# Optimization experiments

Hardware: AMD Instinct MI355X
Metric: run time of the kernel (lower is better)

The kernel has to match this reference:

```python
import jax, jax.numpy as jnp
import numpy as np

B, S, D, H, HD, I, L = 1, 2048, 1024, 16, 64, 2816, 2
EPS = 1e-5
ROPE_BASE = 10000.0


def rmsnorm(x, w):
    return x * jax.lax.rsqrt(jnp.mean(x * x, axis=-1, keepdims=True) + EPS) * w


def precompute_freqs_cis():
    # matches precompute_freqs_cis: [S, HD//2, 2] = (cos, sin)
    freqs = 1.0 / (ROPE_BASE ** (jnp.arange(0, HD, 2, dtype=jnp.float32) / HD))
    ang = jnp.outer(jnp.arange(S, dtype=jnp.float32), freqs)
    return jnp.stack([jnp.cos(ang), jnp.sin(ang)], axis=-1)


def apply_rope(x, fc):
    # x: [B,S,H,HD]; fc: [S,HD//2,2] -> interleaved pair rotation
    xs = x.reshape(*x.shape[:-1], HD // 2, 2)
    f = fc[None, :, None]  # [1,S,1,HD//2,2]
    out = jnp.stack([
        xs[..., 0] * f[..., 0] - xs[..., 1] * f[..., 1],
        xs[..., 1] * f[..., 0] + xs[..., 0] * f[..., 1],
    ], axis=-1)
    return out.reshape(x.shape)


def setup_inputs() -> dict:
    key = jax.random.key(0)
    ks = jax.random.split(key, 6)
    p = lambda k, shape: jax.random.normal(k, shape, jnp.float32) * 0.02
    return {
        "x": jax.random.normal(ks[0], (B, S, D), jnp.float32),
        "wqkv": p(ks[1], (L, 3 * H * HD, D)),
        "wo": p(ks[2], (L, D, H * HD)),
        "w1": p(ks[3], (L, I, D)),
        "w2": p(ks[4], (L, D, I)),
        "w3": p(ks[5], (L, I, D)),
        "attn_norm_w": jnp.ones((L, D), jnp.float32),
        "ffn_norm_w": jnp.ones((L, D), jnp.float32),
        "attn_ls": 0.01 * jnp.ones((L, D), jnp.float32),
        "ffn_ls": 0.01 * jnp.ones((L, D), jnp.float32),
        "final_norm_w": jnp.ones((D,), jnp.float32),
    }


def reference(x, wqkv, wo, w1, w2, w3, attn_norm_w, ffn_norm_w, attn_ls, ffn_ls, final_norm_w):
    fc = precompute_freqs_cis()
    causal = jnp.tril(jnp.ones((S, S), dtype=bool))  # [S,S]
    scale = 1.0 / np.sqrt(HD).astype(np.float32)
    h = x
    for l in range(L):
        # --- attention block ---
        xn = rmsnorm(h, attn_norm_w[l])
        qkv = xn @ wqkv[l].T  # [B,S,3*H*HD]
        q, k, v = jnp.split(qkv, 3, axis=-1)
        q = apply_rope(q.reshape(B, S, H, HD), fc)
        k = apply_rope(k.reshape(B, S, H, HD), fc)
        v = v.reshape(B, S, H, HD)
        scores = jnp.einsum('bqhd,bkhd->bhqk', q, k) * scale
        scores = jnp.where(causal, scores, jnp.finfo(scores.dtype).min)
        attn = jax.nn.softmax(scores, axis=-1)
        y = jnp.einsum('bhqk,bkhd->bqhd', attn, v).reshape(B, S, H * HD)
        h = h + (y @ wo[l].T) * attn_ls[l]
        # --- feed-forward block (SwiGLU) ---
        xn = rmsnorm(h, ffn_norm_w[l])
        ff = (jax.nn.silu(xn @ w1[l].T) * (xn @ w3[l].T)) @ w2[l].T
        h = h + ff * ffn_ls[l]
    return rmsnorm(h, final_norm_w)
```

## Files before the change

### kernel.cpp

```cpp
#include <hip/hip_runtime.h>
#include <math.h>

#define SEQ 2048
#define DIM 1024
#define NH 16
#define HDIM 64
#define IDIM 2816
#define NL 2

typedef __attribute__((ext_vector_type(8))) short bf16x8;
typedef __attribute__((ext_vector_type(4))) float f32x4;

__device__ __forceinline__ unsigned short f2bf(float f) {
    unsigned int u = __float_as_uint(f);
    u = (u + 0x7fffu + ((u >> 16) & 1u)) >> 16;
    return (unsigned short)u;
}
__device__ __forceinline__ float bf2f(unsigned short u) {
    return __uint_as_float((unsigned int)u << 16);
}

__device__ __forceinline__ void gl_lds16(const void* g, void* l) {
    __builtin_amdgcn_global_load_lds(
        (const __attribute__((address_space(1))) unsigned int*)g,
        (__attribute__((address_space(3))) unsigned int*)l, 16, 0, 0);
}

#define WAITVM(n) asm volatile("s_waitcnt vmcnt(" #n ")" ::: "memory")
#define BARRIER_PIN()                       \
    do {                                    \
        __builtin_amdgcn_s_barrier();       \
        __builtin_amdgcn_sched_barrier(0);  \
    } while (0)

template <bool BF16OUT>
__global__ __launch_bounds__(256) void rmsnorm_kernel(const float* __restrict__ in,
                                                      const float* __restrict__ w,
                                                      void* __restrict__ out) {
    const int row = blockIdx.x;
    const int t = threadIdx.x;
    const float4 v = ((const float4*)(in + (size_t)row * DIM))[t];
    float ss = v.x * v.x + v.y * v.y + v.z * v.z + v.w * v.w;
#pragma unroll
    for (int m = 1; m < 64; m <<= 1) ss += __shfl_xor(ss, m);
    __shared__ float red[4];
    if ((t & 63) == 0) red[t >> 6] = ss;
    __syncthreads();
    const float tot = red[0] + red[1] + red[2] + red[3];
    const float r = 1.0f / sqrtf(tot * (1.0f / DIM) + 1e-5f);
    const float4 wv = ((const float4*)w)[t];
    float o0 = v.x * r * wv.x, o1 = v.y * r * wv.y;
    float o2 = v.z * r * wv.z, o3 = v.w * r * wv.w;
    if (BF16OUT) {
        ushort4 o = {f2bf(o0), f2bf(o1), f2bf(o2), f2bf(o3)};
        ((ushort4*)((unsigned short*)out + (size_t)row * DIM))[t] = o;
    } else {
        float4 o = {o0, o1, o2, o3};
        ((float4*)((float*)out + (size_t)row * DIM))[t] = o;
    }
}

#define WQKV_OFF 0
#define WO_OFF   3145728
#define W1_OFF   4194304
#define W3_OFF   7077888
#define W2_OFF   9961472
#define WTOT     12845056

__global__ __launch_bounds__(256) void convert_weights_kernel(
    const float* __restrict__ wqkv, const float* __restrict__ wo,
    const float* __restrict__ w1, const float* __restrict__ w3,
    const float* __restrict__ w2, unsigned short* __restrict__ out) {
    const size_t i8 = ((size_t)blockIdx.x * 256 + threadIdx.x) * 8;
    const float* src;
    size_t local;
    if (i8 < WO_OFF)      { src = wqkv; local = i8 - WQKV_OFF; }
    else if (i8 < W1_OFF) { src = wo;   local = i8 - WO_OFF; }
    else if (i8 < W3_OFF) { src = w1;   local = i8 - W1_OFF; }
    else if (i8 < W2_OFF) { src = w3;   local = i8 - W3_OFF; }
    else                  { src = w2;   local = i8 - W2_OFF; }
    const float4 v0 = *(const float4*)(src + local);
    const float4 v1 = *(const float4*)(src + local + 4);
    ushort4 o0 = {f2bf(v0.x), f2bf(v0.y), f2bf(v0.z), f2bf(v0.w)};
    ushort4 o1 = {f2bf(v1.x), f2bf(v1.y), f2bf(v1.z), f2bf(v1.w)};
    *(ushort4*)(out + i8) = o0;
    *(ushort4*)(out + i8 + 4) = o1;
}

template <int EPI, int BM, int BN, int KSPLIT>
__global__ __launch_bounds__(256) void mfma_gemm(
    const unsigned short* __restrict__ A,
    const unsigned short* __restrict__ B,
    const unsigned short* __restrict__ Bhi, int nsplit,
    float* __restrict__ Cf,
    unsigned short* __restrict__ Cb,
    const float* __restrict__ ls,
    int N, int K) {
    constexpr int MI = BM / 32;
    constexpr int NJ = BN / 32;
    constexpr int L = BM / 64 + BN / 64;
    __shared__ unsigned short As[3][BM * 32];
    __shared__ unsigned short Bs[3][BN * 32];

    const int tid = threadIdx.x;

    const int nwg = gridDim.x * gridDim.y;
    const int orig = blockIdx.y * gridDim.x + blockIdx.x;
    const int swz = (orig & 7) * (nwg >> 3) + (orig >> 3);
    const int bx = swz % gridDim.x;
    const int by = swz / gridDim.x;
    const int m0 = by * BM;
    const int ncol0 = bx * BN;

    const unsigned short* Bp = B;
    int n0 = ncol0;
    if (n0 >= nsplit) { Bp = Bhi; n0 -= nsplit; }

    const int Koff = (KSPLIT > 1) ? blockIdx.z * (K / KSPLIT) : 0;

    const int srow = tid >> 2;
    const int skof = (tid & 3) * 8;
    const unsigned short* Ag = A + (size_t)(m0 + srow) * K + Koff + skof;
    const unsigned short* Bg = Bp + (size_t)(n0 + srow) * K + Koff + skof;

    const int lane = tid & 63;
    const int wid = tid >> 6;
    const int wr = (wid >> 1) * (BM / 2);
    const int wc = (wid & 1) * (BN / 2);
    const int fr = lane & 15;
    const int fk = (lane >> 4) * 8;

    f32x4 acc[MI][NJ] = {};

#define STAGE(buf, kk)                                                        \
    {                                                                         \
        _Pragma("unroll")                                                     \
        for (int p = 0; p < BM / 64; ++p)                                     \
            gl_lds16(Ag + (size_t)(p * 64) * K + (kk),                        \
                     &As[buf][p * 2048 + tid * 8]);                           \
        _Pragma("unroll")                                                     \
        for (int p = 0; p < BN / 64; ++p)                                     \
            gl_lds16(Bg + (size_t)(p * 64) * K + (kk),                        \
                     &Bs[buf][p * 2048 + tid * 8]);                           \
    }

    auto compute_tile = [&](int buf) {
        bf16x8 a[MI], b[NJ];
#pragma unroll
        for (int m = 0; m < MI; ++m)
            a[m] = *(const bf16x8*)&As[buf][(wr + m * 16 + fr) * 32 + fk];
#pragma unroll
        for (int n = 0; n < NJ; ++n)
            b[n] = *(const bf16x8*)&Bs[buf][(wc + n * 16 + fr) * 32 + fk];
        __builtin_amdgcn_s_setprio(1);
#pragma unroll
        for (int m = 0; m < MI; ++m)
#pragma unroll
            for (int n = 0; n < NJ; ++n)
                acc[m][n] = __builtin_amdgcn_mfma_f32_16x16x32_bf16(a[m], b[n], acc[m][n], 0, 0, 0);
        __builtin_amdgcn_s_setprio(0);
    };

    const int NT = K / KSPLIT / 32;

    STAGE(0, 0);
    STAGE(1, 32);
    STAGE(2, 64);

    int buf = 0;
    for (int t = 0; t < NT - 2; ++t) {
        if constexpr (L == 3) WAITVM(6); else WAITVM(8);
        BARRIER_PIN();
        compute_tile(buf);
        asm volatile("s_waitcnt lgkmcnt(0)" ::: "memory");
        BARRIER_PIN();
        if (t + 3 < NT) STAGE(buf, (t + 3) * 32);
        buf = (buf == 2) ? 0 : buf + 1;
    }
    if constexpr (L == 3) WAITVM(3); else WAITVM(4);
    BARRIER_PIN();
    compute_tile(buf);
    asm volatile("s_waitcnt lgkmcnt(0)" ::: "memory");
    BARRIER_PIN();
    buf = (buf == 2) ? 0 : buf + 1;
    WAITVM(0);
    BARRIER_PIN();
    compute_tile(buf);
#undef STAGE

    const int erow = m0 + wr + (lane >> 4) * 4;
    const int ecol = ncol0 + wc + fr;
#pragma unroll
    for (int m = 0; m < MI; ++m) {
#pragma unroll
        for (int n = 0; n < NJ; ++n) {
            const f32x4 v = acc[m][n];
            const int row = erow + m * 16;
            const int col = ecol + n * 16;
            if (EPI == 1) {
                const float lv = ls[col];
#pragma unroll
                for (int j = 0; j < 4; ++j) {
                    float* p = Cf + (size_t)(row + j) * N + col;
                    if (KSPLIT > 1) atomicAdd(p, v[j] * lv);
                    else            *p = *p + v[j] * lv;
                }
            } else {
#pragma unroll
                for (int j = 0; j < 4; ++j)
                    Cb[(size_t)(row + j) * N + col] = f2bf(v[j]);
            }
        }
    }
}

__global__ __launch_bounds__(256) void silu_mul_kernel(
    const unsigned short* __restrict__ c13,
    unsigned short* __restrict__ outp) {
    const size_t e8 = ((size_t)blockIdx.x * 256 + threadIdx.x) * 8;
    const int m = (int)(e8 / IDIM);
    const int i = (int)(e8 % IDIM);
    const unsigned short* g = c13 + (size_t)m * (2 * IDIM) + i;
    const bf16x8 gv = *(const bf16x8*)g;
    const bf16x8 uv = *(const bf16x8*)(g + IDIM);
    unsigned short o[8];
#pragma unroll
    for (int j = 0; j < 8; ++j) {
        const float x = bf2f((unsigned short)gv[j]);
        const float u = bf2f((unsigned short)uv[j]);
        o[j] = f2bf(x / (1.0f + __expf(-x)) * u);
    }
    *(bf16x8*)(outp + (size_t)m * IDIM + i) = *(const bf16x8*)o;
}

__global__ __launch_bounds__(256) void rope_split_kernel(
    const unsigned short* __restrict__ qkv,
    unsigned short* __restrict__ Qh,
    unsigned short* __restrict__ Kh,
    unsigned short* __restrict__ Vt) {
    const int st = blockIdx.x;
    const int h = blockIdx.y;
    const int tid = threadIdx.x;
    const int srow = tid >> 2;
    const int scol = (tid & 3) * 16;
    const int s = st * 64 + srow;
    __shared__ unsigned short Vl[64][72];

    const unsigned short* base = qkv + (size_t)s * (3 * DIM) + h * HDIM + scol;

    unsigned short qv[16], kv[16], vv[16];
    *(bf16x8*)&qv[0] = *(const bf16x8*)(base);
    *(bf16x8*)&qv[8] = *(const bf16x8*)(base + 8);
    *(bf16x8*)&kv[0] = *(const bf16x8*)(base + DIM);
    *(bf16x8*)&kv[8] = *(const bf16x8*)(base + DIM + 8);
    *(bf16x8*)&vv[0] = *(const bf16x8*)(base + 2 * DIM);
    *(bf16x8*)&vv[8] = *(const bf16x8*)(base + 2 * DIM + 8);

    unsigned short qo[16], ko[16];
#pragma unroll
    for (int i = 0; i < 8; ++i) {
        const int p = scol / 2 + i;
        const float freq = powf(10000.0f, -(float)(2 * p) * (1.0f / 64.0f));
        const float ang = (float)s * freq;
        float sn, cs;
        sincosf(ang, &sn, &cs);
        const float q0 = bf2f(qv[2 * i]), q1 = bf2f(qv[2 * i + 1]);
        const float k0 = bf2f(kv[2 * i]), k1 = bf2f(kv[2 * i + 1]);
        qo[2 * i]     = f2bf(q0 * cs - q1 * sn);
        qo[2 * i + 1] = f2bf(q1 * cs + q0 * sn);
        ko[2 * i]     = f2bf(k0 * cs - k1 * sn);
        ko[2 * i + 1] = f2bf(k1 * cs + k0 * sn);
    }
    unsigned short* qdst = Qh + ((size_t)h * SEQ + s) * HDIM + scol;
    unsigned short* kdst = Kh + ((size_t)h * SEQ + s) * HDIM + scol;
    *(bf16x8*)qdst = *(const bf16x8*)&qo[0];
    *(bf16x8*)(qdst + 8) = *(const bf16x8*)&qo[8];
    *(bf16x8*)kdst = *(const bf16x8*)&ko[0];
    *(bf16x8*)(kdst + 8) = *(const bf16x8*)&ko[8];

#pragma unroll
    for (int i = 0; i < 16; ++i) Vl[scol + i][srow] = vv[i];
    __syncthreads();
    const int d = tid >> 2;
    const int c0 = (tid & 3) * 16;
    unsigned short* vdst = Vt + ((size_t)h * HDIM + d) * SEQ + st * 64 + c0;
    *(bf16x8*)vdst = *(const bf16x8*)&Vl[d][c0];
    *(bf16x8*)(vdst + 8) = *(const bf16x8*)&Vl[d][c0 + 8];
}

__global__ __launch_bounds__(256) void attn_mfma_kernel(
    const unsigned short* __restrict__ Qh,
    const unsigned short* __restrict__ Kh,
    const unsigned short* __restrict__ Vt,
    unsigned short* __restrict__ y) {
    const int h = blockIdx.x;
    const int qt = blockIdx.y;
    const int qb = (qt < 16) ? qt : 47 - qt;

    __shared__ unsigned short Ql[64][72];
    __shared__ unsigned short Kl[2][64][72];
    __shared__ unsigned short Vl[2][64][72];
    __shared__ unsigned short Pl[64][72];

    const int tid = threadIdx.x;
    const int lane = tid & 63;
    const int w = tid >> 6;
    const int fr = lane & 15;
    const int fk = (lane >> 4) * 8;
    const int rg = (lane >> 4) * 4;
    const int srow = tid >> 2;
    const int sc8 = (tid & 3) * 8;

    {
        const unsigned short* src = Qh + ((size_t)h * SEQ + qb * 64 + srow) * HDIM + sc8;
        *(bf16x8*)&Ql[srow][sc8] = *(const bf16x8*)src;
        *(bf16x8*)&Ql[srow][sc8 + 32] = *(const bf16x8*)(src + 32);
    }
    __syncthreads();
    bf16x8 qa[2];
    qa[0] = *(const bf16x8*)&Ql[w * 16 + fr][fk];
    qa[1] = *(const bf16x8*)&Ql[w * 16 + fr][32 + fk];

    bf16x8 kr0, kr1, vr0, vr1;
    {
        const unsigned short* ks = Kh + ((size_t)h * SEQ + srow) * HDIM + sc8;
        kr0 = *(const bf16x8*)ks;
        kr1 = *(const bf16x8*)(ks + 32);
        const unsigned short* vs = Vt + ((size_t)h * HDIM + srow) * SEQ + sc8;
        vr0 = *(const bf16x8*)vs;
        vr1 = *(const bf16x8*)(vs + 32);
    }

    float l_[4] = {0.0f, 0.0f, 0.0f, 0.0f};
    f32x4 O[4] = {};

    for (int kb = 0; kb <= qb; ++kb) {
        const int cur = kb & 1;
        *(bf16x8*)&Kl[cur][srow][sc8] = kr0;
        *(bf16x8*)&Kl[cur][srow][sc8 + 32] = kr1;
        *(bf16x8*)&Vl[cur][srow][sc8] = vr0;
        *(bf16x8*)&Vl[cur][srow][sc8 + 32] = vr1;
        __syncthreads();

        if (kb < qb) {
            const unsigned short* ks = Kh + ((size_t)h * SEQ + (kb + 1) * 64 + srow) * HDIM + sc8;
            kr0 = *(const bf16x8*)ks;
            kr1 = *(const bf16x8*)(ks + 32);
            const unsigned short* vs = Vt + ((size_t)h * HDIM + srow) * SEQ + (kb + 1) * 64 + sc8;
            vr0 = *(const bf16x8*)vs;
            vr1 = *(const bf16x8*)(vs + 32);
        }

        f32x4 sa[4] = {};
        __builtin_amdgcn_s_setprio(1);
#pragma unroll
        for (int ks2 = 0; ks2 < 2; ++ks2)
#pragma unroll
            for (int n = 0; n < 4; ++n) {
                const bf16x8 kf = *(const bf16x8*)&Kl[cur][n * 16 + fr][ks2 * 32 + fk];
                sa[n] = __builtin_amdgcn_mfma_f32_16x16x32_bf16(qa[ks2], kf, sa[n], 0, 0, 0);
            }
        __builtin_amdgcn_s_setprio(0);

        const bool diag = (kb == qb);
#pragma unroll
        for (int n = 0; n < 4; ++n) {
            const int col = n * 16 + fr;
#pragma unroll
            for (int j = 0; j < 4; ++j) {
                const float sv = sa[n][j] * 0.125f;
                float e = __expf(fminf(sv, 30.0f));
                if (diag && col > rg + j) e = 0.0f;
                l_[j] += e;
                Pl[w * 16 + rg + j][col] = f2bf(e);
            }
        }

        __builtin_amdgcn_s_setprio(1);
#pragma unroll
        for (int ks2 = 0; ks2 < 2; ++ks2) {
            const bf16x8 pa = *(const bf16x8*)&Pl[w * 16 + fr][ks2 * 32 + fk];
#pragma unroll
            for (int nd = 0; nd < 4; ++nd) {
                const bf16x8 vf = *(const bf16x8*)&Vl[cur][nd * 16 + fr][ks2 * 32 + fk];
                O[nd] = __builtin_amdgcn_mfma_f32_16x16x32_bf16(pa, vf, O[nd], 0, 0, 0);
            }
        }
        __builtin_amdgcn_s_setprio(0);
    }

#pragma unroll
    for (int j = 0; j < 4; ++j) {
#pragma unroll
        for (int msk = 1; msk < 16; msk <<= 1) l_[j] += __shfl_xor(l_[j], msk);
    }

#pragma unroll
    for (int j = 0; j < 4; ++j) {
        const float inv = 1.0f / l_[j];
        unsigned short* dst = y + (size_t)(qb * 64 + w * 16 + rg + j) * DIM + h * HDIM + fr;
#pragma unroll
        for (int nd = 0; nd < 4; ++nd)
            dst[nd * 16] = f2bf(O[nd][j] * inv);
    }
}

extern "C" void kernel_launch(void* const* d_in, const int* in_sizes, int n_in,
                              void* d_out, int out_size, void* d_ws, size_t ws_size,
                              hipStream_t stream) {
    const float* x            = (const float*)d_in[0];
    const float* wqkv         = (const float*)d_in[1];
    const float* wo           = (const float*)d_in[2];
    const float* w1           = (const float*)d_in[3];
    const float* w2           = (const float*)d_in[4];
    const float* w3           = (const float*)d_in[5];
    const float* attn_norm_w  = (const float*)d_in[6];
    const float* ffn_norm_w   = (const float*)d_in[7];
    const float* attn_ls      = (const float*)d_in[8];
    const float* ffn_ls       = (const float*)d_in[9];
    const float* final_norm_w = (const float*)d_in[10];
    float* out = (float*)d_out;

    char* ws = (char*)d_ws;
    float*          h     = (float*)ws;
    unsigned short* xnb   = (unsigned short*)(ws + 8388608);
    unsigned short* yb    = (unsigned short*)(ws + 12582912);
    unsigned short* qkvb  = (unsigned short*)(ws + 16777216);
    unsigned short* Qhb   = (unsigned short*)(ws + 29360128);
    unsigned short* Khb   = (unsigned short*)(ws + 33554432);
    unsigned short* Vtb   = (unsigned short*)(ws + 37748736);
    unsigned short* c13   = (unsigned short*)(ws + 16777216);
    unsigned short* ffb   = (unsigned short*)(ws + 41943040);
    unsigned short* wbuf  = (unsigned short*)(ws + 46137344);

    unsigned short* wqkv_b = wbuf + WQKV_OFF;
    unsigned short* wo_b   = wbuf + WO_OFF;
    unsigned short* w1_b   = wbuf + W1_OFF;
    unsigned short* w3_b   = wbuf + W3_OFF;
    unsigned short* w2_b   = wbuf + W2_OFF;

    const int BIG = 1 << 30;

    hipMemcpyAsync(h, x, (size_t)SEQ * DIM * sizeof(float),
                   hipMemcpyDeviceToDevice, stream);

    for (int l = 0; l < NL; ++l) {
        convert_weights_kernel<<<WTOT / 2048, 256, 0, stream>>>(
            wqkv + (size_t)l * 3 * DIM * DIM, wo + (size_t)l * DIM * DIM,
            w1 + (size_t)l * IDIM * DIM, w3 + (size_t)l * IDIM * DIM,
            w2 + (size_t)l * DIM * IDIM, wbuf);

        rmsnorm_kernel<true><<<SEQ, 256, 0, stream>>>(h, attn_norm_w + l * DIM, xnb);
        mfma_gemm<3, 64, 128, 1><<<dim3(3 * DIM / 128, SEQ / 64), 256, 0, stream>>>(
            xnb, wqkv_b, nullptr, BIG, nullptr, qkvb, nullptr, 3 * DIM, DIM);
        rope_split_kernel<<<dim3(SEQ / 64, NH), 256, 0, stream>>>(qkvb, Qhb, Khb, Vtb);
        attn_mfma_kernel<<<dim3(NH, SEQ / 64), 256, 0, stream>>>(Qhb, Khb, Vtb, yb);
        mfma_gemm<1, 64, 128, 2><<<dim3(DIM / 128, SEQ / 64, 2), 256, 0, stream>>>(
            yb, wo_b, nullptr, BIG, h, nullptr, attn_ls + l * DIM, DIM, DIM);

        rmsnorm_kernel<true><<<SEQ, 256, 0, stream>>>(h, ffn_norm_w + l * DIM, xnb);
        mfma_gemm<3, 128, 128, 1><<<dim3(2 * IDIM / 128, SEQ / 128), 256, 0, stream>>>(
            xnb, w1_b, w3_b, IDIM, nullptr, c13, nullptr, 2 * IDIM, DIM);
        silu_mul_kernel<<<SEQ * IDIM / 2048, 256, 0, stream>>>(c13, ffb);
        mfma_gemm<1, 64, 128, 4><<<dim3(DIM / 128, SEQ / 64, 4), 256, 0, stream>>>(
            ffb, w2_b, nullptr, BIG, h, nullptr, ffn_ls + l * DIM, DIM, IDIM);
    }

    rmsnorm_kernel<false><<<SEQ, 256, 0, stream>>>(h, final_norm_w, out);
}
```

Baseline: 387.8 us.

## Fuse SiLU-gate multiply into dual-B W1/W3 GEMM and swizzle LDS layout

The W1 and W3 GEMM now loads both weight tiles into shared memory and keeps two accumulators per output tile, applying silu(g)*u in the epilogue. This removes the separate silu_mul kernel and the round trip of the 2*IDIM bf16 intermediate through global memory. The GEMM also XOR-swizzles the k-offset in the LDS staging and fragment reads of every tile to reduce bank conflicts. In exchange the fused kernel uses more LDS and registers per block and runs with 64x128 tiles instead of 128x128, so it issues more A loads.

```diff
diff --git a/kernel.cpp b/kernel.cpp
--- a/kernel.cpp
+++ b/kernel.cpp
@@ -98,9 +98,11 @@
     int N, int K) {
     constexpr int MI = BM / 32;
     constexpr int NJ = BN / 32;
-    constexpr int L = BM / 64 + BN / 64;
+    constexpr int L = BM / 64 + BN / 64 + ((EPI == 2) ? BN / 64 : 0);
+    static_assert(L == 3 || L == 5, "WAITVM literals cover L=3,5 only");
     __shared__ unsigned short As[3][BM * 32];
     __shared__ unsigned short Bs[3][BN * 32];
+    __shared__ unsigned short B2s[(EPI == 2) ? 3 : 1][(EPI == 2) ? BN * 32 : 8];
 
     const int tid = threadIdx.x;
 
@@ -119,39 +121,44 @@
     const int Koff = (KSPLIT > 1) ? blockIdx.z * (K / KSPLIT) : 0;
 
     const int srow = tid >> 2;
-    const int skof = (tid & 3) * 8;
+    const int skof = (((tid & 3) ^ ((tid >> 3) & 3)) << 3);
     const unsigned short* Ag = A + (size_t)(m0 + srow) * K + Koff + skof;
     const unsigned short* Bg = Bp + (size_t)(n0 + srow) * K + Koff + skof;
+    const unsigned short* B2g =
+        (EPI == 2) ? Bhi + (size_t)(n0 + srow) * K + Koff + skof : nullptr;
 
     const int lane = tid & 63;
     const int wid = tid >> 6;
     const int wr = (wid >> 1) * (BM / 2);
     const int wc = (wid & 1) * (BN / 2);
     const int fr = lane & 15;
-    const int fk = (lane >> 4) * 8;
+    const int fkx = (((lane >> 4) ^ ((fr >> 1) & 3)) << 3);
 
     f32x4 acc[MI][NJ] = {};
-
-#define STAGE(buf, kk)                                                        \
-    {                                                                         \
-        _Pragma("unroll")                                                     \
-        for (int p = 0; p < BM / 64; ++p)                                     \
-            gl_lds16(Ag + (size_t)(p * 64) * K + (kk),                        \
-                     &As[buf][p * 2048 + tid * 8]);                           \
-        _Pragma("unroll")                                                     \
-        for (int p = 0; p < BN / 64; ++p)                                     \
-            gl_lds16(Bg + (size_t)(p * 64) * K + (kk),                        \
-                     &Bs[buf][p * 2048 + tid * 8]);                           \
-    }
+    f32x4 acc2[(EPI == 2) ? MI : 1][NJ] = {};
+
+    auto stage = [&](int buf, int kk) {
+#pragma unroll
+        for (int p = 0; p < BM / 64; ++p)
+            gl_lds16(Ag + (size_t)(p * 64) * K + kk, &As[buf][p * 2048 + tid * 8]);
+#pragma unroll
+        for (int p = 0; p < BN / 64; ++p)
+            gl_lds16(Bg + (size_t)(p * 64) * K + kk, &Bs[buf][p * 2048 + tid * 8]);
+        if constexpr (EPI == 2) {
+#pragma unroll
+            for (int p = 0; p < BN / 64; ++p)
+                gl_lds16(B2g + (size_t)(p * 64) * K + kk, &B2s[buf][p * 2048 + tid * 8]);
+        }
+    };
 
     auto compute_tile = [&](int buf) {
         bf16x8 a[MI], b[NJ];
 #pragma unroll
         for (int m = 0; m < MI; ++m)
-            a[m] = *(const bf16x8*)&As[buf][(wr + m * 16 + fr) * 32 + fk];
+            a[m] = *(const bf16x8*)&As[buf][(wr + m * 16 + fr) * 32 + fkx];
 #pragma unroll
         for (int n = 0; n < NJ; ++n)
-            b[n] = *(const bf16x8*)&Bs[buf][(wc + n * 16 + fr) * 32 + fk];
+            b[n] = *(const bf16x8*)&Bs[buf][(wc + n * 16 + fr) * 32 + fkx];
         __builtin_amdgcn_s_setprio(1);
 #pragma unroll
         for (int m = 0; m < MI; ++m)
@@ -159,25 +166,38 @@
             for (int n = 0; n < NJ; ++n)
                 acc[m][n] = __builtin_amdgcn_mfma_f32_16x16x32_bf16(a[m], b[n], acc[m][n], 0, 0, 0);
         __builtin_amdgcn_s_setprio(0);
+        if constexpr (EPI == 2) {
+            bf16x8 c[NJ];
+#pragma unroll
+            for (int n = 0; n < NJ; ++n)
+                c[n] = *(const bf16x8*)&B2s[buf][(wc + n * 16 + fr) * 32 + fkx];
+            __builtin_amdgcn_s_setprio(1);
+#pragma unroll
+            for (int m = 0; m < MI; ++m)
+#pragma unroll
+                for (int n = 0; n < NJ; ++n)
+                    acc2[m][n] = __builtin_amdgcn_mfma_f32_16x16x32_bf16(a[m], c[n], acc2[m][n], 0, 0, 0);
+            __builtin_amdgcn_s_setprio(0);
+        }
     };
 
     const int NT = K / KSPLIT / 32;
 
-    STAGE(0, 0);
-    STAGE(1, 32);
-    STAGE(2, 64);
+    stage(0, 0);
+    stage(1, 32);
+    stage(2, 64);
 
     int buf = 0;
     for (int t = 0; t < NT - 2; ++t) {
-        if constexpr (L == 3) WAITVM(6); else WAITVM(8);
+        if constexpr (L == 3) WAITVM(6); else WAITVM(10);
         BARRIER_PIN();
         compute_tile(buf);
         asm volatile("s_waitcnt lgkmcnt(0)" ::: "memory");
         BARRIER_PIN();
-        if (t + 3 < NT) STAGE(buf, (t + 3) * 32);
+        if (t + 3 < NT) stage(buf, (t + 3) * 32);
         buf = (buf == 2) ? 0 : buf + 1;
     }
-    if constexpr (L == 3) WAITVM(3); else WAITVM(4);
+    if constexpr (L == 3) WAITVM(3); else WAITVM(5);
     BARRIER_PIN();
     compute_tile(buf);
     asm volatile("s_waitcnt lgkmcnt(0)" ::: "memory");
@@ -186,7 +206,6 @@
     WAITVM(0);
     BARRIER_PIN();
     compute_tile(buf);
-#undef STAGE
 
     const int erow = m0 + wr + (lane >> 4) * 4;
     const int ecol = ncol0 + wc + fr;
@@ -205,6 +224,14 @@
                     if (KSPLIT > 1) atomicAdd(p, v[j] * lv);
                     else            *p = *p + v[j] * lv;
                 }
+            } else if (EPI == 2) {
+                const f32x4 v2 = acc2[m][n];
+#pragma unroll
+                for (int j = 0; j < 4; ++j) {
+                    const float g = v[j];
+                    Cb[(size_t)(row + j) * N + col] =
+                        f2bf(g / (1.0f + __expf(-g)) * v2[j]);
+                }
             } else {
 #pragma unroll
                 for (int j = 0; j < 4; ++j)
@@ -212,25 +239,6 @@
             }
         }
     }
-}
-
-__global__ __launch_bounds__(256) void silu_mul_kernel(
-    const unsigned short* __restrict__ c13,
-    unsigned short* __restrict__ outp) {
-    const size_t e8 = ((size_t)blockIdx.x * 256 + threadIdx.x) * 8;
-    const int m = (int)(e8 / IDIM);
-    const int i = (int)(e8 % IDIM);
-    const unsigned short* g = c13 + (size_t)m * (2 * IDIM) + i;
-    const bf16x8 gv = *(const bf16x8*)g;
-    const bf16x8 uv = *(const bf16x8*)(g + IDIM);
-    unsigned short o[8];
-#pragma unroll
-    for (int j = 0; j < 8; ++j) {
-        const float x = bf2f((unsigned short)gv[j]);
-        const float u = bf2f((unsigned short)uv[j]);
-        o[j] = f2bf(x / (1.0f + __expf(-x)) * u);
-    }
-    *(bf16x8*)(outp + (size_t)m * IDIM + i) = *(const bf16x8*)o;
 }
 
 __global__ __launch_bounds__(256) void rope_split_kernel(
@@ -429,7 +437,6 @@
     unsigned short* Qhb   = (unsigned short*)(ws + 29360128);
     unsigned short* Khb   = (unsigned short*)(ws + 33554432);
     unsigned short* Vtb   = (unsigned short*)(ws + 37748736);
-    unsigned short* c13   = (unsigned short*)(ws + 16777216);
     unsigned short* ffb   = (unsigned short*)(ws + 41943040);
     unsigned short* wbuf  = (unsigned short*)(ws + 46137344);
 
@@ -459,9 +466,8 @@
             yb, wo_b, nullptr, BIG, h, nullptr, attn_ls + l * DIM, DIM, DIM);
 
         rmsnorm_kernel<true><<<SEQ, 256, 0, stream>>>(h, ffn_norm_w + l * DIM, xnb);
-        mfma_gemm<3, 128, 128, 1><<<dim3(2 * IDIM / 128, SEQ / 128), 256, 0, stream>>>(
-            xnb, w1_b, w3_b, IDIM, nullptr, c13, nullptr, 2 * IDIM, DIM);
-        silu_mul_kernel<<<SEQ * IDIM / 2048, 256, 0, stream>>>(c13, ffb);
+        mfma_gemm<2, 64, 128, 1><<<dim3(IDIM / 128, SEQ / 64), 256, 0, stream>>>(
+            xnb, w1_b, w3_b, BIG, nullptr, ffb, nullptr, IDIM, DIM);
         mfma_gemm<1, 64, 128, 4><<<dim3(DIM / 128, SEQ / 64, 4), 256, 0, stream>>>(
             ffb, w2_b, nullptr, BIG, h, nullptr, ffn_ls + l * DIM, DIM, IDIM);
     }
```

New measurement: 420.4 us. 8.4% more time.

## Switch GEMM to BK=64 double-buffered XOR-swizzled LDS tiles

Applied to the files above, without the earlier changes.

The GEMM pipeline moves from a triple-buffered 32-wide K tile to a double-buffered 64-wide K tile, so there are half as many barriers per K. The LDS layout gains an XOR swizzle on 16-byte column chunks to avoid bank conflicts on fragment reads. The w1/w3 GEMM drops from a 128x128 to a 64x128 tile, which raises the workgroup count but lowers data reuse per tile. A static_assert restricts the kernel to 64x128 tiles because the vmcnt wait literals are now hardcoded.

```diff
diff --git a/kernel.cpp b/kernel.cpp
--- a/kernel.cpp
+++ b/kernel.cpp
@@ -98,9 +98,9 @@
     int N, int K) {
     constexpr int MI = BM / 32;
     constexpr int NJ = BN / 32;
-    constexpr int L = BM / 64 + BN / 64;
-    __shared__ unsigned short As[3][BM * 32];
-    __shared__ unsigned short Bs[3][BN * 32];
+    static_assert(BM == 64 && BN == 128, "vmcnt literals sized for 64x128");
+    __shared__ unsigned short As[2][BM * 64];
+    __shared__ unsigned short Bs[2][BN * 64];
 
     const int tid = threadIdx.x;
 
@@ -118,77 +118,83 @@
 
     const int Koff = (KSPLIT > 1) ? blockIdx.z * (K / KSPLIT) : 0;
 
-    const int srow = tid >> 2;
-    const int skof = (tid & 3) * 8;
-    const unsigned short* Ag = A + (size_t)(m0 + srow) * K + Koff + skof;
-    const unsigned short* Bg = Bp + (size_t)(n0 + srow) * K + Koff + skof;
+    const int r0 = tid >> 3;
+    const int cswz = (tid & 7) ^ (r0 & 7);
+    const unsigned short* Ag = A + (size_t)(m0 + r0) * K + Koff + cswz * 8;
+    const unsigned short* Bg = Bp + (size_t)(n0 + r0) * K + Koff + cswz * 8;
 
     const int lane = tid & 63;
     const int wid = tid >> 6;
     const int wr = (wid >> 1) * (BM / 2);
     const int wc = (wid & 1) * (BN / 2);
     const int fr = lane & 15;
-    const int fk = (lane >> 4) * 8;
+    const int hi = lane >> 4;
 
     f32x4 acc[MI][NJ] = {};
 
-#define STAGE(buf, kk)                                                        \
-    {                                                                         \
-        _Pragma("unroll")                                                     \
-        for (int p = 0; p < BM / 64; ++p)                                     \
-            gl_lds16(Ag + (size_t)(p * 64) * K + (kk),                        \
-                     &As[buf][p * 2048 + tid * 8]);                           \
-        _Pragma("unroll")                                                     \
-        for (int p = 0; p < BN / 64; ++p)                                     \
-            gl_lds16(Bg + (size_t)(p * 64) * K + (kk),                        \
-                     &Bs[buf][p * 2048 + tid * 8]);                           \
-    }
+    auto stage = [&](int buf, int kk) {
+#pragma unroll
+        for (int p = 0; p < BM / 64; ++p)
+#pragma unroll
+            for (int i = 0; i < 2; ++i)
+                gl_lds16(Ag + (size_t)(p * 64 + i * 32) * K + kk,
+                         &As[buf][(p * 64 + i * 32) * 64 + tid * 8]);
+#pragma unroll
+        for (int p = 0; p < BN / 64; ++p)
+#pragma unroll
+            for (int i = 0; i < 2; ++i)
+                gl_lds16(Bg + (size_t)(p * 64 + i * 32) * K + kk,
+                         &Bs[buf][(p * 64 + i * 32) * 64 + tid * 8]);
+    };
+
+    auto frag = [&](const unsigned short* base, int R, int c) -> bf16x8 {
+        return *(const bf16x8*)&base[R * 64 + ((c ^ (R & 7)) << 3)];
+    };
 
     auto compute_tile = [&](int buf) {
-        bf16x8 a[MI], b[NJ];
+        bf16x8 a[MI][2], b[NJ][2];
 #pragma unroll
         for (int m = 0; m < MI; ++m)
-            a[m] = *(const bf16x8*)&As[buf][(wr + m * 16 + fr) * 32 + fk];
+#pragma unroll
+            for (int kw = 0; kw < 2; ++kw)
+                a[m][kw] = frag(As[buf], wr + m * 16 + fr, kw * 4 + hi);
 #pragma unroll
         for (int n = 0; n < NJ; ++n)
-            b[n] = *(const bf16x8*)&Bs[buf][(wc + n * 16 + fr) * 32 + fk];
+#pragma unroll
+            for (int kw = 0; kw < 2; ++kw)
+                b[n][kw] = frag(Bs[buf], wc + n * 16 + fr, kw * 4 + hi);
         __builtin_amdgcn_s_setprio(1);
 #pragma unroll
-        for (int m = 0; m < MI; ++m)
-#pragma unroll
-            for (int n = 0; n < NJ; ++n)
-                acc[m][n] = __builtin_amdgcn_mfma_f32_16x16x32_bf16(a[m], b[n], acc[m][n], 0, 0, 0);
+        for (int kw = 0; kw < 2; ++kw)
+#pragma unroll
+            for (int m = 0; m < MI; ++m)
+#pragma unroll
+                for (int n = 0; n < NJ; ++n)
+                    acc[m][n] = __builtin_amdgcn_mfma_f32_16x16x32_bf16(
+                        a[m][kw], b[n][kw], acc[m][n], 0, 0, 0);
         __builtin_amdgcn_s_setprio(0);
     };
 
-    const int NT = K / KSPLIT / 32;
-
-    STAGE(0, 0);
-    STAGE(1, 32);
-    STAGE(2, 64);
+    const int NT = K / KSPLIT / 64;
+
+    stage(0, 0);
+    stage(1, 64);
 
     int buf = 0;
-    for (int t = 0; t < NT - 2; ++t) {
-        if constexpr (L == 3) WAITVM(6); else WAITVM(8);
+    for (int t = 0; t < NT - 1; ++t) {
+        WAITVM(6);
         BARRIER_PIN();
         compute_tile(buf);
         asm volatile("s_waitcnt lgkmcnt(0)" ::: "memory");
         BARRIER_PIN();
-        if (t + 3 < NT) STAGE(buf, (t + 3) * 32);
-        buf = (buf == 2) ? 0 : buf + 1;
-    }
-    if constexpr (L == 3) WAITVM(3); else WAITVM(4);
-    BARRIER_PIN();
-    compute_tile(buf);
-    asm volatile("s_waitcnt lgkmcnt(0)" ::: "memory");
-    BARRIER_PIN();
-    buf = (buf == 2) ? 0 : buf + 1;
+        if (t + 2 < NT) stage(buf, (t + 2) * 64);
+        buf ^= 1;
+    }
     WAITVM(0);
     BARRIER_PIN();
     compute_tile(buf);
-#undef STAGE
-
-    const int erow = m0 + wr + (lane >> 4) * 4;
+
+    const int erow = m0 + wr + hi * 4;
     const int ecol = ncol0 + wc + fr;
 #pragma unroll
     for (int m = 0; m < MI; ++m) {
@@ -459,7 +465,7 @@
             yb, wo_b, nullptr, BIG, h, nullptr, attn_ls + l * DIM, DIM, DIM);
 
         rmsnorm_kernel<true><<<SEQ, 256, 0, stream>>>(h, ffn_norm_w + l * DIM, xnb);
-        mfma_gemm<3, 128, 128, 1><<<dim3(2 * IDIM / 128, SEQ / 128), 256, 0, stream>>>(
+        mfma_gemm<3, 64, 128, 1><<<dim3(2 * IDIM / 128, SEQ / 64), 256, 0, stream>>>(
             xnb, w1_b, w3_b, IDIM, nullptr, c13, nullptr, 2 * IDIM, DIM);
         silu_mul_kernel<<<SEQ * IDIM / 2048, 256, 0, stream>>>(c13, ffb);
         mfma_gemm<1, 64, 128, 4><<<dim3(DIM / 128, SEQ / 64, 4), 256, 0, stream>>>(
```

After: 379.2 us. -2.2%, faster.
